# Performance work log

Hardware: AMD Instinct MI355X
Metric: run time of the kernel (lower is better)

The kernel has to match this reference:

```python
import jax, jax.numpy as jnp
import numpy as np

H = 64
V = 50257
B = 32
L = 4096
LN_EPS = 1e-5
DELTA_EPS = 1e-6


def setup_inputs() -> dict:
    key = jax.random.key(0)
    ks = jax.random.split(key, 10)
    s = 0.02
    return {
        "seq": jax.random.randint(ks[0], (B, L), 0, V),
        "read_pos": -1,
        "embed": jax.random.normal(ks[1], (V, H), jnp.float32) * s,
        "w1": jax.random.normal(ks[2], (H, 2 * H), jnp.float32) * s,
        "b1": jnp.zeros((2 * H,), jnp.float32),
        "w2": jax.random.normal(ks[3], (2 * H, H), jnp.float32) * s,
        "b2": jnp.zeros((H,), jnp.float32),
        "ln_g": jnp.ones((H,), jnp.float32),
        "ln_b": jnp.zeros((H,), jnp.float32),
        "rp_w": jax.random.normal(ks[4], (H, H), jnp.float32) * s,
        "rp_b": jnp.zeros((H,), jnp.float32),
        "out_w": jax.random.normal(ks[5], (H, V), jnp.float32) * s,
        "out_b": jnp.zeros((V,), jnp.float32),
    }


def _encoder(seq, embed, w1, b1, w2, b2, ln_g, ln_b):
    e = embed[seq]  # [B, L, H]
    f = jnp.maximum(e @ w1 + b1, 0.0) @ w2 + b2  # FFN
    x = e + f
    mu = jnp.mean(x, axis=-1, keepdims=True)
    var = jnp.mean((x - mu) ** 2, axis=-1, keepdims=True)
    return (x - mu) * jax.lax.rsqrt(var + LN_EPS) * ln_g + ln_b


def _delta_memory(h_all):
    # Strictly sequential delta-rule fast-weight update over t = 0..L-2.
    Bs, Ls, Hs = h_all.shape
    keys = jnp.transpose(h_all[:, : Ls - 1, :], (1, 0, 2))  # [L-1, B, H]

    def step(M, k):
        vp = jnp.einsum('bij,bj->bi', M, k)  # M @ k
        u = k - vp / (jnp.sum(k * k, axis=-1, keepdims=True) + DELTA_EPS)
        M = M + u[:, :, None] * k[:, None, :]  # outer product update
        return M, None

    M0 = jnp.zeros((Bs, Hs, Hs), h_all.dtype)
    M, _ = jax.lax.scan(step, M0, keys)
    return M


def reference(seq, read_pos, embed, w1, b1, w2, b2, ln_g, ln_b, rp_w, rp_b, out_w, out_b):
    h_all = _encoder(seq, embed, w1, b1, w2, b2, ln_g, ln_b)  # [B, L, H]
    M = _delta_memory(h_all)  # [B, H, H]
    q = h_all[:, read_pos, :]  # [B, H]
    r = jnp.einsum('bij,bj->bi', M, q)
    return (r @ rp_w + rp_b) @ out_w + out_b  # [B, V]
```

## Files before the change

kernel.cpp:

```cpp
#include <hip/hip_runtime.h>

#define HH 64
#define VV 50257
#define BB 32
#define LL 4096

constexpr float LN_EPS_F = 1e-5f;
constexpr float DELTA_EPS_F = 1e-6f;

constexpr int CS = 64;
constexpr int NG = LL / CS;

typedef float f32x4 __attribute__((ext_vector_type(4)));
typedef float f32x2 __attribute__((ext_vector_type(2)));
typedef short bf16x8 __attribute__((ext_vector_type(8)));
union U16x8 { uint4 u; bf16x8 v; unsigned short s[8]; };

__device__ __forceinline__ unsigned short f2bf(float f) {
  union { float f; unsigned u; } v; v.f = f;
  unsigned r = v.u + 0x7fff + ((v.u >> 16) & 1);
  return (unsigned short)(r >> 16);
}

__device__ __forceinline__ unsigned cvt_pk_bf16(float a, float b) {
  unsigned r;
  asm("v_cvt_pk_bf16_f32 %0, %1, %2" : "=v"(r) : "v"(a), "v"(b));
  return r;
}

__device__ __forceinline__ void split2(float a, float b, unsigned& hp, unsigned& lp) {
  hp = cvt_pk_bf16(a, b);
  float ha = __uint_as_float(hp << 16);
  float hb = __uint_as_float(hp & 0xffff0000u);
  lp = cvt_pk_bf16(a - ha, b - hb);
}

template <int CTRL>
__device__ __forceinline__ float dpp_add(float x) {
  int t = __builtin_amdgcn_update_dpp(0, __float_as_int(x), CTRL, 0xF, 0xF, true);
  return x + __int_as_float(t);
}

__device__ __forceinline__ float wave_sum_lane63(float x) {
  x = dpp_add<0x111>(x);
  x = dpp_add<0x112>(x);
  x = dpp_add<0x114>(x);
  x = dpp_add<0x118>(x);
  x = dpp_add<0x142>(x);
  x = dpp_add<0x143>(x);
  return x;
}

__device__ __forceinline__ float readlane_f(float x, int lane) {
  return __int_as_float(__builtin_amdgcn_readlane(__float_as_int(x), lane));
}

__global__ __launch_bounds__(256) void prep_kernel(
    const float* __restrict__ w1, const float* __restrict__ w2,
    unsigned short* __restrict__ w1b, unsigned short* __restrict__ w2b) {
  int i = blockIdx.x * 256 + threadIdx.x;
  if (i < 8192) {
    int jj = i >> 6, h = i & 63;
    w1b[i] = f2bf(w1[h * 128 + jj]);
  } else {
    int k = i - 8192;
    int h = k >> 7, jj = k & 127;
    w2b[k] = f2bf(w2[jj * 64 + h]);
  }
}

__global__ __launch_bounds__(64, 1) void encoder_kernel(
    const int* __restrict__ seq, const float* __restrict__ embed,
    const unsigned short* __restrict__ w1b, const float* __restrict__ b1,
    const unsigned short* __restrict__ w2b, const float* __restrict__ b2,
    const float* __restrict__ ln_g, const float* __restrict__ ln_b,
    float* __restrict__ h_all, float* __restrict__ beta) {
  __shared__ __align__(16) char pool[26624];
  unsigned short (*e_l)[72] = reinterpret_cast<unsigned short (*)[72]>(pool);
  unsigned short (*act_l)[136] = reinterpret_cast<unsigned short (*)[136]>(pool + 9216);
  float (*x_l)[65] = reinterpret_cast<float (*)[65]>(pool);
  __shared__ float2 gb_l[64];
  __shared__ float b1_l[128], b2_l[64];

  int lane = threadIdx.x;
  int q = lane >> 4, l = lane & 15;
  int base = blockIdx.x * 64;
  int s = seq[base + lane];

  {
    const float4* ep = reinterpret_cast<const float4*>(embed + (size_t)s * HH);
#pragma unroll
    for (int i = 0; i < 8; ++i) {
      float4 va = ep[2 * i], vb = ep[2 * i + 1];
      uint4 u;
      u.x = cvt_pk_bf16(va.x, va.y);
      u.y = cvt_pk_bf16(va.z, va.w);
      u.z = cvt_pk_bf16(vb.x, vb.y);
      u.w = cvt_pk_bf16(vb.z, vb.w);
      *(uint4*)&e_l[lane][8 * i] = u;
    }
  }
  gb_l[lane] = make_float2(ln_g[lane], ln_b[lane]);
  b1_l[lane] = b1[lane];
  b1_l[64 + lane] = b1[64 + lane];
  b2_l[lane] = b2[lane];

  bf16x8 af1[8][2];
#pragma unroll
  for (int mi = 0; mi < 8; ++mi)
#pragma unroll
    for (int ks = 0; ks < 2; ++ks) {
      U16x8 t;
      t.u = *(const uint4*)(w1b + (mi * 16 + l) * 64 + ks * 32 + q * 8);
      af1[mi][ks] = t.v;
    }

  __syncthreads();

  f32x4 acc1[8][4];
#pragma unroll
  for (int mi = 0; mi < 8; ++mi)
#pragma unroll
    for (int nt = 0; nt < 4; ++nt) acc1[mi][nt] = (f32x4){0.f, 0.f, 0.f, 0.f};

#pragma unroll
  for (int ks = 0; ks < 2; ++ks) {
    bf16x8 bfr[4];
#pragma unroll
    for (int nt = 0; nt < 4; ++nt) {
      U16x8 t;
      t.u = *(const uint4*)&e_l[nt * 16 + l][ks * 32 + q * 8];
      bfr[nt] = t.v;
    }
#pragma unroll
    for (int mi = 0; mi < 8; ++mi)
#pragma unroll
      for (int nt = 0; nt < 4; ++nt)
        acc1[mi][nt] = __builtin_amdgcn_mfma_f32_16x16x32_bf16(
            af1[mi][ks], bfr[nt], acc1[mi][nt], 0, 0, 0);
  }

#pragma unroll
  for (int mi = 0; mi < 8; ++mi)
#pragma unroll
    for (int nt = 0; nt < 4; ++nt) {
      int tok = nt * 16 + l;
      int jj0 = mi * 16 + q * 4;
      float v0 = fmaxf(acc1[mi][nt][0] + b1_l[jj0 + 0], 0.f);
      float v1 = fmaxf(acc1[mi][nt][1] + b1_l[jj0 + 1], 0.f);
      float v2 = fmaxf(acc1[mi][nt][2] + b1_l[jj0 + 2], 0.f);
      float v3 = fmaxf(acc1[mi][nt][3] + b1_l[jj0 + 3], 0.f);
      uint2 u;
      u.x = cvt_pk_bf16(v0, v1);
      u.y = cvt_pk_bf16(v2, v3);
      *(uint2*)&act_l[tok][jj0] = u;
    }

  bf16x8 bf2[4][4];
#pragma unroll
  for (int nt = 0; nt < 4; ++nt)
#pragma unroll
    for (int ks = 0; ks < 4; ++ks) {
      U16x8 t;
      t.u = *(const uint4*)(w2b + (nt * 16 + l) * 128 + ks * 32 + q * 8);
      bf2[nt][ks] = t.v;
    }

  __syncthreads();

  f32x4 acc2[4][4];
#pragma unroll
  for (int mt = 0; mt < 4; ++mt)
#pragma unroll
    for (int nt = 0; nt < 4; ++nt) acc2[mt][nt] = (f32x4){0.f, 0.f, 0.f, 0.f};

#pragma unroll
  for (int ks = 0; ks < 4; ++ks) {
    bf16x8 afr[4];
#pragma unroll
    for (int mt = 0; mt < 4; ++mt) {
      U16x8 t;
      t.u = *(const uint4*)&act_l[mt * 16 + l][ks * 32 + q * 8];
      afr[mt] = t.v;
    }
#pragma unroll
    for (int mt = 0; mt < 4; ++mt)
#pragma unroll
      for (int nt = 0; nt < 4; ++nt)
        acc2[mt][nt] = __builtin_amdgcn_mfma_f32_16x16x32_bf16(
            afr[mt], bf2[nt][ks], acc2[mt][nt], 0, 0, 0);
  }

  __syncthreads();

#pragma unroll
  for (int mt = 0; mt < 4; ++mt)
#pragma unroll
    for (int nt = 0; nt < 4; ++nt) {
      int h = nt * 16 + l;
#pragma unroll
      for (int r = 0; r < 4; ++r) {
        int tok = mt * 16 + q * 4 + r;
        x_l[tok][h] = acc2[mt][nt][r] + b2_l[h];
      }
    }

  __syncthreads();

  float x[HH];
#pragma unroll
  for (int h = 0; h < HH; ++h) x[h] = x_l[lane][h];
  {
    const float4* ep = reinterpret_cast<const float4*>(embed + (size_t)s * HH);
#pragma unroll
    for (int i = 0; i < 16; ++i) {
      float4 v = ep[i];
      x[4 * i + 0] += v.x; x[4 * i + 1] += v.y;
      x[4 * i + 2] += v.z; x[4 * i + 3] += v.w;
    }
  }
  float sum = 0.f;
#pragma unroll
  for (int h = 0; h < HH; ++h) sum += x[h];
  float mu = sum * (1.f / HH);
  float vs = 0.f;
#pragma unroll
  for (int h = 0; h < HH; ++h) { float dx = x[h] - mu; vs = fmaf(dx, dx, vs); }
  float rstd = rsqrtf(vs * (1.f / HH) + LN_EPS_F);

  float ss = 0.f;
#pragma unroll
  for (int h = 0; h < HH; ++h) {
    float2 gb = gb_l[h];
    float o = fmaf((x[h] - mu) * rstd, gb.x, gb.y);
    ss = fmaf(o, o, ss);
    x[h] = o;
  }
  float4* hp = reinterpret_cast<float4*>(h_all + (size_t)(base + lane) * HH);
#pragma unroll
  for (int i = 0; i < 16; ++i)
    hp[i] = make_float4(x[4 * i + 0], x[4 * i + 1], x[4 * i + 2], x[4 * i + 3]);
  beta[base + lane] = 1.f / (ss + DELTA_EPS_F);
}

__global__ __launch_bounds__(64, 1) void gram_n_kernel(
    const float* __restrict__ h_all, const float* __restrict__ beta,
    float* __restrict__ Ng) {
  __shared__ __align__(16) char smem[27136];
  unsigned short (*pA)[64][72] = reinterpret_cast<unsigned short (*)[64][72]>(smem);
  float* Glp = reinterpret_cast<float*>(smem + 18432);
  char* pBh0 = smem + 18432;
  float* bl = reinterpret_cast<float*>(smem + 26880);

  int c = blockIdx.x, b = blockIdx.y, lane = threadIdx.x;
  int q = lane >> 4, l = lane & 15;
  const float* src = h_all + ((size_t)b * LL + c * CS) * HH;

  bf16x8 ah[2][4], al_[2][4];
#pragma unroll
  for (int ks = 0; ks < 2; ++ks)
#pragma unroll
    for (int i = 0; i < 4; ++i) {
      const float* p = src + (i * 16 + l) * 64 + ks * 32 + q * 8;
      float4 va = *(const float4*)p, vb = *(const float4*)(p + 4);
      U16x8 hi, lo;
      split2(va.x, va.y, hi.u.x, lo.u.x);
      split2(va.z, va.w, hi.u.y, lo.u.y);
      split2(vb.x, vb.y, hi.u.z, lo.u.z);
      split2(vb.z, vb.w, hi.u.w, lo.u.w);
      ah[ks][i] = hi.v; al_[ks][i] = lo.v;
    }
  if (c == NG - 1 && l == 15) {
#pragma unroll
    for (int ks = 0; ks < 2; ++ks) {
      ah[ks][3] = (bf16x8){0, 0, 0, 0, 0, 0, 0, 0};
      al_[ks][3] = (bf16x8){0, 0, 0, 0, 0, 0, 0, 0};
    }
  }

  bl[lane] = beta[(size_t)b * LL + c * CS + lane];

  f32x2 m2[32];
#pragma unroll
  for (int t = 0; t < 32; ++t)
    m2[t] = (f32x2){src[(2 * t) * 64 + lane], src[(2 * t + 1) * 64 + lane]};
  if (c == NG - 1) m2[31].y = 0.f;

  f32x4 acc[4][4];
#pragma unroll
  for (int mi = 0; mi < 4; ++mi)
#pragma unroll
    for (int nt = 0; nt <= mi; ++nt) acc[mi][nt] = (f32x4){0.f, 0.f, 0.f, 0.f};

#pragma unroll
  for (int ks = 0; ks < 2; ++ks)
#pragma unroll
    for (int mi = 0; mi < 4; ++mi)
#pragma unroll
      for (int nt = 0; nt <= mi; ++nt) {
        acc[mi][nt] = __builtin_amdgcn_mfma_f32_16x16x32_bf16(ah[ks][mi], ah[ks][nt], acc[mi][nt], 0, 0, 0);
        acc[mi][nt] = __builtin_amdgcn_mfma_f32_16x16x32_bf16(ah[ks][mi], al_[ks][nt], acc[mi][nt], 0, 0, 0);
        acc[mi][nt] = __builtin_amdgcn_mfma_f32_16x16x32_bf16(al_[ks][mi], ah[ks][nt], acc[mi][nt], 0, 0, 0);
      }

#pragma unroll
  for (int mi = 0; mi < 4; ++mi) {
    int gg = 4 * mi + q;
    int e1 = 8 * gg * (gg + 1);
    int o0 = 4 * gg * (2 * gg + 1);
    int o1 = e1;
    int o2 = e1 + 4 * (gg + 1);
    int o3 = e1 + 8 * (gg + 1);
#pragma unroll
    for (int nt = 0; nt < mi; ++nt) {
      int t = nt * 16 + l;
      Glp[o0 + t] = acc[mi][nt][0];
      Glp[o1 + t] = acc[mi][nt][1];
      Glp[o2 + t] = acc[mi][nt][2];
      Glp[o3 + t] = acc[mi][nt][3];
    }
    {
      int t = mi * 16 + l;
      if (l < 4 * q)     Glp[o0 + t] = acc[mi][mi][0];
      if (l < 4 * q + 1) Glp[o1 + t] = acc[mi][mi][1];
      if (l < 4 * q + 2) Glp[o2 + t] = acc[mi][mi][2];
      if (l < 4 * q + 3) Glp[o3 + t] = acc[mi][mi][3];
    }
  }

#pragma unroll
  for (int i = 0; i < 16; ++i) {
    unsigned h0, l0, h1, l1;
    split2(m2[2 * i].x, m2[2 * i].y, h0, l0);
    split2(m2[2 * i + 1].x, m2[2 * i + 1].y, h1, l1);
    *(uint2*)&pA[0][lane][4 * i] = make_uint2(h0, h1);
    *(uint2*)&pA[1][lane][4 * i] = make_uint2(l0, l1);
  }
  __syncthreads();

#pragma unroll
  for (int g = 15; g >= 0; --g) {
    int e1 = 8 * g * (g + 1);
    int o0 = 4 * g * (2 * g + 1);
    int o1 = e1;
    int o2 = e1 + 4 * (g + 1);
    int o3 = e1 + 8 * (g + 1);
    float4 C1 = *(const float4*)(Glp + o1 + 4 * g);
    float4 C2 = *(const float4*)(Glp + o2 + 4 * g);
    float4 C3 = *(const float4*)(Glp + o3 + 4 * g);
    float4 B4 = *(const float4*)(bl + 4 * g);

    float t3 = B4.w * m2[2 * g + 1].y;
    float v2 = fmaf(-C3.z, t3, m2[2 * g + 1].x);
    float t2 = B4.z * v2;
    float v1 = fmaf(-C2.y, t2, fmaf(-C3.y, t3, m2[2 * g].y));
    float t1 = B4.y * v1;
    float v0 = fmaf(-C1.x, t1, fmaf(-C2.x, t2, fmaf(-C3.x, t3, m2[2 * g].x)));
    float t0 = B4.x * v0;
    m2[2 * g] = (f32x2){t0, t1};
    m2[2 * g + 1] = (f32x2){t2, t3};
    f32x2 n0 = {-t0, -t0}, n1 = {-t1, -t1}, n2 = {-t2, -t2}, n3 = {-t3, -t3};

#pragma unroll
    for (int j = 0; j < g; ++j) {
      float4 R0 = *(const float4*)(Glp + o0 + 4 * j);
      float4 R1 = *(const float4*)(Glp + o1 + 4 * j);
      float4 R2 = *(const float4*)(Glp + o2 + 4 * j);
      float4 R3 = *(const float4*)(Glp + o3 + 4 * j);
      f32x2 a = m2[2 * j], d = m2[2 * j + 1];
      a = __builtin_elementwise_fma((f32x2){R0.x, R0.y}, n0, a);
      a = __builtin_elementwise_fma((f32x2){R1.x, R1.y}, n1, a);
      a = __builtin_elementwise_fma((f32x2){R2.x, R2.y}, n2, a);
      a = __builtin_elementwise_fma((f32x2){R3.x, R3.y}, n3, a);
      d = __builtin_elementwise_fma((f32x2){R0.z, R0.w}, n0, d);
      d = __builtin_elementwise_fma((f32x2){R1.z, R1.w}, n1, d);
      d = __builtin_elementwise_fma((f32x2){R2.z, R2.w}, n2, d);
      d = __builtin_elementwise_fma((f32x2){R3.z, R3.w}, n3, d);
      m2[2 * j] = a; m2[2 * j + 1] = d;
    }
  }

  __syncthreads();

  f32x4 acc2[4][4];
#pragma unroll
  for (int mi = 0; mi < 4; ++mi)
#pragma unroll
    for (int nt = 0; nt < 4; ++nt) acc2[mi][nt] = (f32x4){0.f, 0.f, 0.f, 0.f};

#pragma unroll
  for (int hf = 0; hf < 2; ++hf) {
#pragma unroll
    for (int i2 = 0; i2 < 8; ++i2) {
      int tt = hf * 16 + 2 * i2;
      unsigned h0, l0, h1, l1;
      split2(m2[tt].x, m2[tt].y, h0, l0);
      split2(m2[tt + 1].x, m2[tt + 1].y, h1, l1);
      unsigned boff = (unsigned)((lane * 64 + i2 * 8) ^ ((lane & 7) << 4));
      *(uint2*)(pBh0 + boff) = make_uint2(h0, h1);
      *(uint2*)(pBh0 + 4096 + boff) = make_uint2(l0, l1);
    }
    __syncthreads();

    bf16x8 kh[4], kl_[4], bh[4], blo[4];
#pragma unroll
    for (int i = 0; i < 4; ++i) {
      U16x8 t;
      t.u = *(const uint4*)&pA[0][i * 16 + l][hf * 32 + q * 8]; kh[i] = t.v;
      t.u = *(const uint4*)&pA[1][i * 16 + l][hf * 32 + q * 8]; kl_[i] = t.v;
      unsigned bro = (unsigned)((((16 * i + l) * 64) + q * 16) ^ ((l & 7) << 4));
      t.u = *(const uint4*)(pBh0 + bro);        bh[i] = t.v;
      t.u = *(const uint4*)(pBh0 + 4096 + bro); blo[i] = t.v;
    }
#pragma unroll
    for (int mi = 0; mi < 4; ++mi)
#pragma unroll
      for (int nt = 0; nt < 4; ++nt) {
        acc2[mi][nt] = __builtin_amdgcn_mfma_f32_16x16x32_bf16(kh[mi], bh[nt], acc2[mi][nt], 0, 0, 0);
        acc2[mi][nt] = __builtin_amdgcn_mfma_f32_16x16x32_bf16(kh[mi], blo[nt], acc2[mi][nt], 0, 0, 0);
        acc2[mi][nt] = __builtin_amdgcn_mfma_f32_16x16x32_bf16(kl_[mi], bh[nt], acc2[mi][nt], 0, 0, 0);
      }
    __syncthreads();
  }

  float* np = Ng + (((size_t)b * NG + c) << 12);
#pragma unroll
  for (int mi = 0; mi < 4; ++mi)
#pragma unroll
    for (int nt = 0; nt < 4; ++nt) {
      int h0 = mi * 16 + q * 4, hp = nt * 16 + l;
      float4 v;
      v.x = ((h0 + 0 == hp) ? 1.f : 0.f) - acc2[mi][nt][0];
      v.y = ((h0 + 1 == hp) ? 1.f : 0.f) - acc2[mi][nt][1];
      v.z = ((h0 + 2 == hp) ? 1.f : 0.f) - acc2[mi][nt][2];
      v.w = ((h0 + 3 == hp) ? 1.f : 0.f) - acc2[mi][nt][3];
      *(float4*)&np[hp * 64 + h0] = v;
    }
}

__global__ __launch_bounds__(64, 1) void boundary_kernel(
    const float* __restrict__ h_all, const float* __restrict__ Ng,
    const int* __restrict__ read_pos_p, float* __restrict__ Qg) {
  __shared__ __align__(16) float nt0[64 * 64];
  __shared__ __align__(16) float nt1[64 * 64];
  __shared__ __align__(16) float ql[64];

  int b = blockIdx.x, lane = threadIdx.x;
  int rpv = read_pos_p[0];
  int pos = rpv < 0 ? rpv + LL : rpv;
  float Q = h_all[((size_t)b * LL + pos) * HH + lane];

  const float* Nb = Ng + ((size_t)b * NG << 12);

  auto load_chunk = [&](float* buf, int c) {
    const float* g = Nb + ((size_t)c << 12);
#pragma unroll
    for (int i = 0; i < 16; ++i)
      __builtin_amdgcn_global_load_lds(
          (const __attribute__((address_space(1))) unsigned*)(g + i * 256 + lane * 4),
          (__attribute__((address_space(3))) unsigned*)(buf + i * 256), 16, 0, 0);
  };

  auto step = [&](const float* buf, int c, bool last) {
    if (last) __builtin_amdgcn_s_waitcnt(0x0F70);
    else      __builtin_amdgcn_s_waitcnt(0x4F70);
    Qg[((size_t)b * NG + c) * HH + lane] = Q;
    ql[lane] = Q;
    float a0 = 0.f, a1 = 0.f, a2 = 0.f, a3 = 0.f;
#pragma unroll
    for (int j = 0; j < 64; j += 4) {
      float4 q4 = *(const float4*)&ql[j];
      a0 = fmaf(buf[(j + 0) * 64 + lane], q4.x, a0);
      a1 = fmaf(buf[(j + 1) * 64 + lane], q4.y, a1);
      a2 = fmaf(buf[(j + 2) * 64 + lane], q4.z, a2);
      a3 = fmaf(buf[(j + 3) * 64 + lane], q4.w, a3);
    }
    Q = (a0 + a1) + (a2 + a3);
  };

  load_chunk(nt1, NG - 1);
  load_chunk(nt0, NG - 2);

#pragma unroll 1
  for (int c = NG - 1; c >= 1; c -= 2) {
    step(nt1, c, false);
    __builtin_amdgcn_s_waitcnt(0xC07F);
    if (c >= 3) load_chunk(nt1, c - 2);
    step(nt0, c - 1, c == 1);
    __builtin_amdgcn_s_waitcnt(0xC07F);
    if (c >= 3) load_chunk(nt0, c - 3);
  }
}

__global__ __launch_bounds__(64, 1) void chunk_scan_kernel(
    const float* __restrict__ h_all, const float* __restrict__ beta,
    const float* __restrict__ Qg, float* __restrict__ rc) {
  int c = blockIdx.x, b = blockIdx.y, j = threadIdx.x;
  const float* hb = h_all + (size_t)b * LL * HH;
  const float* betab = beta + (size_t)b * LL;

  float P = Qg[((size_t)b * NG + c) * HH + j];
  float r = 0.f;

  float kk[CS];
#pragma unroll
  for (int i = 0; i < CS; ++i) kk[i] = hb[((size_t)(c * CS + i)) * HH + j];
  float bv = betab[c * CS + j];

  bool last = (c == NG - 1);
#pragma unroll
  for (int i = CS - 1; i >= 0; --i) {
    float k = kk[i];
    float bt = readlane_f(bv, i);
    float m = k * P;
    float s = wave_sum_lane63(m);
    float d = readlane_f(s, 63);
    if (i == CS - 1 && last) d = 0.f;
    r = fmaf(d, k, r);
    P = fmaf(-(bt * d), k, P);
  }
  rc[((size_t)b * NG + c) * HH + j] = r;
}

__global__ __launch_bounds__(64, 1) void combine_kernel(
    const float* __restrict__ rc, const float* __restrict__ rp_w,
    const float* __restrict__ rp_b, float* __restrict__ yv) {
  int b = blockIdx.x, j = threadIdx.x;
  float r = 0.f;
#pragma unroll 8
  for (int cc = 0; cc < NG; ++cc) r += rc[((size_t)b * NG + cc) * HH + j];
  __shared__ float rs[HH];
  rs[j] = r;
  __syncthreads();
  float yj = rp_b[j];
#pragma unroll
  for (int h = 0; h < HH; ++h) yj = fmaf(rs[h], rp_w[h * HH + j], yj);
  yv[b * HH + j] = yj;
}

__global__ __launch_bounds__(256, 2) void out_kernel(
    const float* __restrict__ yv, const float* __restrict__ out_w,
    const float* __restrict__ out_b, float* __restrict__ out) {
  __shared__ float ys[BB * HH];
  for (int i = threadIdx.x; i < BB * HH; i += 256) ys[i] = yv[i];
  __syncthreads();

  int v = blockIdx.x * 256 + threadIdx.x;
  if (v >= VV) return;

  float acc[BB];
  float ob = out_b[v];
#pragma unroll
  for (int b = 0; b < BB; ++b) acc[b] = ob;

  for (int h = 0; h < HH; ++h) {
    float w = out_w[(size_t)h * VV + v];
#pragma unroll
    for (int b = 0; b < BB; ++b) acc[b] = fmaf(ys[b * HH + h], w, acc[b]);
  }
#pragma unroll
  for (int b = 0; b < BB; ++b) out[(size_t)b * VV + v] = acc[b];
}

extern "C" void kernel_launch(void* const* d_in, const int* in_sizes, int n_in,
                              void* d_out, int out_size, void* d_ws, size_t ws_size,
                              hipStream_t stream) {
  (void)in_sizes; (void)n_in; (void)out_size; (void)ws_size;
  const int*   seq   = (const int*)d_in[0];
  const int*   rp    = (const int*)d_in[1];
  const float* embed = (const float*)d_in[2];
  const float* w1    = (const float*)d_in[3];
  const float* b1    = (const float*)d_in[4];
  const float* w2    = (const float*)d_in[5];
  const float* b2    = (const float*)d_in[6];
  const float* ln_g  = (const float*)d_in[7];
  const float* ln_b  = (const float*)d_in[8];
  const float* rp_w  = (const float*)d_in[9];
  const float* rp_b  = (const float*)d_in[10];
  const float* out_w = (const float*)d_in[11];
  const float* out_b = (const float*)d_in[12];
  float* out = (float*)d_out;

  float* h_all = (float*)d_ws;
  float* beta  = h_all + (size_t)BB * LL * HH;
  float* Ng    = beta + (size_t)BB * LL;
  float* Qg    = Ng + (size_t)BB * NG * HH * HH;
  float* rcv   = Qg + (size_t)BB * NG * HH;
  float* yv    = rcv + (size_t)BB * NG * HH;
  unsigned short* w1b = (unsigned short*)(yv + (size_t)BB * HH);
  unsigned short* w2b = w1b + 8192;

  prep_kernel<<<64, 256, 0, stream>>>(w1, w2, w1b, w2b);
  encoder_kernel<<<BB * LL / 64, 64, 0, stream>>>(seq, embed, w1b, b1, w2b, b2,
                                                  ln_g, ln_b, h_all, beta);
  gram_n_kernel<<<dim3(NG, BB), 64, 0, stream>>>(h_all, beta, Ng);
  boundary_kernel<<<BB, 64, 0, stream>>>(h_all, Ng, rp, Qg);
  chunk_scan_kernel<<<dim3(NG, BB), 64, 0, stream>>>(h_all, beta, Qg, rcv);
  combine_kernel<<<BB, 64, 0, stream>>>(rcv, rp_w, rp_b, yv);
  out_kernel<<<(VV + 255) / 256, 256, 0, stream>>>(yv, out_w, out_b, out);
}
```

Before: 235.3 us.

## Shrink LDS in encoder and gram kernels to raise occupancy

The encoder now stages the ReLU activations in 32-column chunks interleaved with the second GEMM's k-steps, which cuts its LDS pool from 26.6KB to 16.6KB at the cost of extra barriers. The gram_n kernel drops the shared bf16 hi/lo copy of the keys (pA) and instead reloads the key columns from global memory, splitting them in registers. A special case zeroes the final key of the last chunk. LDS per block falls to about 8.7KB and launch bounds allow 2 blocks per CU, trading redundant global reads and register pressure for more resident waves.

```diff
diff --git a/kernel.cpp b/kernel.cpp
--- a/kernel.cpp
+++ b/kernel.cpp
@@ -75,9 +75,9 @@
     const unsigned short* __restrict__ w2b, const float* __restrict__ b2,
     const float* __restrict__ ln_g, const float* __restrict__ ln_b,
     float* __restrict__ h_all, float* __restrict__ beta) {
-  __shared__ __align__(16) char pool[26624];
+  __shared__ __align__(16) char pool[16640];
   unsigned short (*e_l)[72] = reinterpret_cast<unsigned short (*)[72]>(pool);
-  unsigned short (*act_l)[136] = reinterpret_cast<unsigned short (*)[136]>(pool + 9216);
+  unsigned short (*chunk)[40] = reinterpret_cast<unsigned short (*)[40]>(pool + 9216);
   float (*x_l)[65] = reinterpret_cast<float (*)[65]>(pool);
   __shared__ float2 gb_l[64];
   __shared__ float b1_l[128], b2_l[64];
@@ -140,22 +140,6 @@
             af1[mi][ks], bfr[nt], acc1[mi][nt], 0, 0, 0);
   }
 
-#pragma unroll
-  for (int mi = 0; mi < 8; ++mi)
-#pragma unroll
-    for (int nt = 0; nt < 4; ++nt) {
-      int tok = nt * 16 + l;
-      int jj0 = mi * 16 + q * 4;
-      float v0 = fmaxf(acc1[mi][nt][0] + b1_l[jj0 + 0], 0.f);
-      float v1 = fmaxf(acc1[mi][nt][1] + b1_l[jj0 + 1], 0.f);
-      float v2 = fmaxf(acc1[mi][nt][2] + b1_l[jj0 + 2], 0.f);
-      float v3 = fmaxf(acc1[mi][nt][3] + b1_l[jj0 + 3], 0.f);
-      uint2 u;
-      u.x = cvt_pk_bf16(v0, v1);
-      u.y = cvt_pk_bf16(v2, v3);
-      *(uint2*)&act_l[tok][jj0] = u;
-    }
-
   bf16x8 bf2[4][4];
 #pragma unroll
   for (int nt = 0; nt < 4; ++nt)
@@ -166,8 +150,6 @@
       bf2[nt][ks] = t.v;
     }
 
-  __syncthreads();
-
   f32x4 acc2[4][4];
 #pragma unroll
   for (int mt = 0; mt < 4; ++mt)
@@ -175,12 +157,32 @@
     for (int nt = 0; nt < 4; ++nt) acc2[mt][nt] = (f32x4){0.f, 0.f, 0.f, 0.f};
 
 #pragma unroll
-  for (int ks = 0; ks < 4; ++ks) {
+  for (int ks2 = 0; ks2 < 4; ++ks2) {
+#pragma unroll
+    for (int mm = 0; mm < 2; ++mm) {
+      int mi = 2 * ks2 + mm;
+      int jj0 = mi * 16 + q * 4;
+      int col = mm * 16 + q * 4;
+#pragma unroll
+      for (int nt = 0; nt < 4; ++nt) {
+        int tok = nt * 16 + l;
+        float v0 = fmaxf(acc1[mi][nt][0] + b1_l[jj0 + 0], 0.f);
+        float v1 = fmaxf(acc1[mi][nt][1] + b1_l[jj0 + 1], 0.f);
+        float v2 = fmaxf(acc1[mi][nt][2] + b1_l[jj0 + 2], 0.f);
+        float v3 = fmaxf(acc1[mi][nt][3] + b1_l[jj0 + 3], 0.f);
+        uint2 u;
+        u.x = cvt_pk_bf16(v0, v1);
+        u.y = cvt_pk_bf16(v2, v3);
+        *(uint2*)&chunk[tok][col] = u;
+      }
+    }
+    __syncthreads();
+
     bf16x8 afr[4];
 #pragma unroll
     for (int mt = 0; mt < 4; ++mt) {
       U16x8 t;
-      t.u = *(const uint4*)&act_l[mt * 16 + l][ks * 32 + q * 8];
+      t.u = *(const uint4*)&chunk[mt * 16 + l][q * 8];
       afr[mt] = t.v;
     }
 #pragma unroll
@@ -188,10 +190,9 @@
 #pragma unroll
       for (int nt = 0; nt < 4; ++nt)
         acc2[mt][nt] = __builtin_amdgcn_mfma_f32_16x16x32_bf16(
-            afr[mt], bf2[nt][ks], acc2[mt][nt], 0, 0, 0);
-  }
-
-  __syncthreads();
+            afr[mt], bf2[nt][ks2], acc2[mt][nt], 0, 0, 0);
+    __syncthreads();
+  }
 
 #pragma unroll
   for (int mt = 0; mt < 4; ++mt)
@@ -243,14 +244,13 @@
   beta[base + lane] = 1.f / (ss + DELTA_EPS_F);
 }
 
-__global__ __launch_bounds__(64, 1) void gram_n_kernel(
+__global__ __launch_bounds__(64, 2) void gram_n_kernel(
     const float* __restrict__ h_all, const float* __restrict__ beta,
     float* __restrict__ Ng) {
-  __shared__ __align__(16) char smem[27136];
-  unsigned short (*pA)[64][72] = reinterpret_cast<unsigned short (*)[64][72]>(smem);
-  float* Glp = reinterpret_cast<float*>(smem + 18432);
-  char* pBh0 = smem + 18432;
-  float* bl = reinterpret_cast<float*>(smem + 26880);
+  __shared__ __align__(16) char smem[8704];
+  float* Glp = reinterpret_cast<float*>(smem);
+  char* pBh0 = smem;
+  float* bl = reinterpret_cast<float*>(smem + 8448);
 
   int c = blockIdx.x, b = blockIdx.y, lane = threadIdx.x;
   int q = lane >> 4, l = lane & 15;
@@ -326,15 +326,6 @@
       if (l < 4 * q + 2) Glp[o2 + t] = acc[mi][mi][2];
       if (l < 4 * q + 3) Glp[o3 + t] = acc[mi][mi][3];
     }
-  }
-
-#pragma unroll
-  for (int i = 0; i < 16; ++i) {
-    unsigned h0, l0, h1, l1;
-    split2(m2[2 * i].x, m2[2 * i].y, h0, l0);
-    split2(m2[2 * i + 1].x, m2[2 * i + 1].y, h1, l1);
-    *(uint2*)&pA[0][lane][4 * i] = make_uint2(h0, h1);
-    *(uint2*)&pA[1][lane][4 * i] = make_uint2(l0, l1);
   }
   __syncthreads();
 
@@ -390,6 +381,13 @@
 
 #pragma unroll
   for (int hf = 0; hf < 2; ++hf) {
+    float av[4][8];
+#pragma unroll
+    for (int mi = 0; mi < 4; ++mi)
+#pragma unroll
+      for (int r = 0; r < 8; ++r)
+        av[mi][r] = src[(hf * 32 + q * 8 + r) * 64 + mi * 16 + l];
+
 #pragma unroll
     for (int i2 = 0; i2 < 8; ++i2) {
       int tt = hf * 16 + 2 * i2;
@@ -402,23 +400,37 @@
     }
     __syncthreads();
 
-    bf16x8 kh[4], kl_[4], bh[4], blo[4];
+    if (c == NG - 1 && hf == 1 && q == 3) {
+      av[0][7] = 0.f; av[1][7] = 0.f; av[2][7] = 0.f; av[3][7] = 0.f;
+    }
+
+    bf16x8 ka[4], kl2[4];
+#pragma unroll
+    for (int mi = 0; mi < 4; ++mi) {
+      U16x8 hi, lo;
+      split2(av[mi][0], av[mi][1], hi.u.x, lo.u.x);
+      split2(av[mi][2], av[mi][3], hi.u.y, lo.u.y);
+      split2(av[mi][4], av[mi][5], hi.u.z, lo.u.z);
+      split2(av[mi][6], av[mi][7], hi.u.w, lo.u.w);
+      ka[mi] = hi.v; kl2[mi] = lo.v;
+    }
+
+    bf16x8 bh[4], blo[4];
 #pragma unroll
     for (int i = 0; i < 4; ++i) {
+      unsigned bro = (unsigned)((((16 * i + l) * 64) + q * 16) ^ ((l & 7) << 4));
       U16x8 t;
-      t.u = *(const uint4*)&pA[0][i * 16 + l][hf * 32 + q * 8]; kh[i] = t.v;
-      t.u = *(const uint4*)&pA[1][i * 16 + l][hf * 32 + q * 8]; kl_[i] = t.v;
-      unsigned bro = (unsigned)((((16 * i + l) * 64) + q * 16) ^ ((l & 7) << 4));
       t.u = *(const uint4*)(pBh0 + bro);        bh[i] = t.v;
       t.u = *(const uint4*)(pBh0 + 4096 + bro); blo[i] = t.v;
     }
+
 #pragma unroll
     for (int mi = 0; mi < 4; ++mi)
 #pragma unroll
       for (int nt = 0; nt < 4; ++nt) {
-        acc2[mi][nt] = __builtin_amdgcn_mfma_f32_16x16x32_bf16(kh[mi], bh[nt], acc2[mi][nt], 0, 0, 0);
-        acc2[mi][nt] = __builtin_amdgcn_mfma_f32_16x16x32_bf16(kh[mi], blo[nt], acc2[mi][nt], 0, 0, 0);
-        acc2[mi][nt] = __builtin_amdgcn_mfma_f32_16x16x32_bf16(kl_[mi], bh[nt], acc2[mi][nt], 0, 0, 0);
+        acc2[mi][nt] = __builtin_amdgcn_mfma_f32_16x16x32_bf16(ka[mi], bh[nt], acc2[mi][nt], 0, 0, 0);
+        acc2[mi][nt] = __builtin_amdgcn_mfma_f32_16x16x32_bf16(ka[mi], blo[nt], acc2[mi][nt], 0, 0, 0);
+        acc2[mi][nt] = __builtin_amdgcn_mfma_f32_16x16x32_bf16(kl2[mi], bh[nt], acc2[mi][nt], 0, 0, 0);
       }
     __syncthreads();
   }
```

After: 221.3 us (median of 3 runs). -5.9%, faster.
